# Kernel optimization log

Measured on AMD Instinct MI355X. Metric: run time of the kernel, lower is better.

## Reference

```python
import jax, jax.numpy as jnp
import numpy as np

B, C, H, W = 8, 64, 64, 64
CQ = C // 8  # query/key channels


def setup_inputs() -> dict:
    key = jax.random.key(0)
    ks = jax.random.split(key, 7)
    s = 0.05
    return {
        "x": jax.random.normal(ks[0], (B, C, H, W), jnp.float32),
        "wq": jax.random.normal(ks[1], (CQ, C), jnp.float32) * s,
        "bq": jnp.zeros((CQ,), jnp.float32),
        "wk": jax.random.normal(ks[2], (CQ, C), jnp.float32) * s,
        "bk": jnp.zeros((CQ,), jnp.float32),
        "wv": jax.random.normal(ks[3], (C, C), jnp.float32) * s,
        "bv": jnp.zeros((C,), jnp.float32),
    }


def reference(x, wq, bq, wk, bk, wv, bv):
    b, c, h, w = x.shape
    n = h * w
    xf = x.reshape(b, c, n)                       # [B, C, N]
    # 1x1 convs == per-pixel linear over channels
    q = jnp.einsum('oc,bcn->bon', wq, xf) + bq[None, :, None]   # [B, CQ, N]
    k = jnp.einsum('oc,bcn->bon', wk, xf) + bk[None, :, None]   # [B, CQ, N]
    v = jnp.einsum('oc,bcn->bon', wv, xf) + bv[None, :, None]   # [B, C, N]
    # energy[b, i, j] = q[b, :, i] . k[b, :, j]  (unscaled)
    energy = jnp.einsum('bci,bcj->bij', q, k)     # [B, N, N]
    attention = jax.nn.softmax(energy, axis=-1)   # softmax over j
    # out[b, c, i] = sum_j v[b, c, j] * attention[b, i, j]
    out = jnp.einsum('bcj,bij->bci', v, attention)
    return out.reshape(b, c, h, w)
```

## Files before the change

kernel.cpp:

```cpp
#include <hip/hip_runtime.h>
#include <hip/hip_bf16.h>


#define B_   8
#define C_   64
#define N_   4096
#define LOG2E 1.44269504088896340736f

typedef short bf16x8 __attribute__((ext_vector_type(8)));
typedef float f32x4  __attribute__((ext_vector_type(4)));
typedef unsigned int uint32;

#if __has_builtin(__builtin_amdgcn_exp2f)
#define EXP2(x) __builtin_amdgcn_exp2f(x)
#else
#define EXP2(x) __expf((x) * 0.69314718055994530942f)
#endif

__device__ __forceinline__ unsigned short f2bf_rn(float f) {
    union { __hip_bfloat16 h; unsigned short u; } cv;
    cv.h = __float2bfloat16(f);
    return cv.u;
}
__device__ __forceinline__ uint32 pk_rn(float lo, float hi) {
    return (uint32)f2bf_rn(lo) | ((uint32)f2bf_rn(hi) << 16);
}
__device__ __forceinline__ uint32 pack_rtz(float lo, float hi) {
    return __builtin_amdgcn_perm(__float_as_uint(hi), __float_as_uint(lo), 0x07060302);
}

__global__ __launch_bounds__(256) void prep_kernel(
    const float* __restrict__ x,
    const float* __restrict__ wq, const float* __restrict__ bq,
    const float* __restrict__ wk, const float* __restrict__ bk,
    unsigned short* __restrict__ Qh, unsigned short* __restrict__ Kh,
    unsigned short* __restrict__ Xb)
{
    __shared__ float Xs[C_][64];
    __shared__ float Wqk[16][C_];
    __shared__ float Bqk[16];

    const int t  = threadIdx.x;
    const int b  = blockIdx.x >> 6;
    const int p0 = (blockIdx.x & 63) << 6;

    for (int i = t; i < 1024; i += 256) {
        int o = i >> 6;
        Wqk[o][i & 63] = (o < 8) ? wq[i] * LOG2E : wk[i - 512];
    }
    if (t < 16) Bqk[t] = (t < 8) ? bq[t] * LOG2E : bk[t - 8];

    for (int i = t; i < 2048; i += 256) {
        int c = i >> 5, p2 = (i & 31) << 1;
        const float* xp = x + ((size_t)b * C_ + c) * N_ + p0 + p2;
        float2 v = *(const float2*)xp;
        Xs[c][p2] = v.x; Xs[c][p2 + 1] = v.y;
        *(uint32*)(Xb + ((size_t)b * C_ + c) * N_ + p0 + p2) = pk_rn(v.x, v.y);
    }
    __syncthreads();

    const int pix = t & 63, grp = t >> 6;
    float a[4];
    #pragma unroll
    for (int r = 0; r < 4; ++r) a[r] = Bqk[grp * 4 + r];
    for (int c = 0; c < C_; ++c) {
        float xv = Xs[c][pix];
        #pragma unroll
        for (int r = 0; r < 4; ++r) a[r] += Wqk[grp * 4 + r][c] * xv;
    }
    #pragma unroll
    for (int r = 0; r < 4; ++r) {
        int o = grp * 4 + r;
        unsigned short hv = f2bf_rn(a[r]);
        if (o < 8) Qh[((size_t)b * N_ + p0 + pix) * 8 + o] = hv;
        else       Kh[((size_t)b * N_ + p0 + pix) * 8 + (o - 8)] = hv;
    }
}

__global__ __launch_bounds__(512, 4) void attn_mfma9_kernel(
    const unsigned short* __restrict__ Qh,
    const unsigned short* __restrict__ Kh,
    const unsigned short* __restrict__ Xb,
    const float* __restrict__ wv, const float* __restrict__ bv,
    float* __restrict__ out)
{
    __shared__ __align__(16) char smem[67584];

    const int t    = threadIdx.x;
    const int w    = t >> 6;
    const int lane = t & 63;
    const int l16  = lane & 15;
    const int qd   = lane >> 4;
    const int p    = w & 3;
    const int h    = w >> 2;
    const int b    = blockIdx.x >> 6;
    const int i0   = (blockIdx.x & 63) << 6;

    const bf16x8 z8 = {};
    const f32x4  zf = {};

    bf16x8 qf[4];
    #pragma unroll
    for (int qt = 0; qt < 4; ++qt) {
        qf[qt] = z8;
        if (qd == 0)
            qf[qt] = *(const bf16x8*)(Qh + ((size_t)b * N_ + i0 + qt * 16 + l16) * 8);
    }

    const unsigned short* Kp = Kh + ((size_t)b * N_ + p * 1024 + h * 16) * 8;
    const unsigned short* Xp = Xb + ((size_t)b * C_ + h * 32) * N_ + p * 1024;

    f32x4 acc[2][4];
    #pragma unroll
    for (int ct = 0; ct < 2; ++ct)
        #pragma unroll
        for (int qt = 0; qt < 4; ++qt) acc[ct][qt] = zf;
    float dsum[4] = {0.f, 0.f, 0.f, 0.f};

    const int swz   = (l16 & 3) << 2;
    const int pbase = p * 8192 + l16 * 64;
    const int woff  = ((h * 8 + qd * 2) ^ swz) << 2;
    const int roff  = ((qd * 4) ^ swz) << 2;

    bf16x8 kf[2], xf[2][2];
    kf[0] = z8;
    if (qd == 0) kf[0] = *(const bf16x8*)(Kp + (size_t)l16 * 8);
    #pragma unroll
    for (int ct = 0; ct < 2; ++ct)
        xf[0][ct] = *(const bf16x8*)(Xp + (size_t)(ct * 16 + l16) * N_ + qd * 8);

    #pragma unroll 2
    for (int s = 0; s < 32; ++s) {
        const int cur = s & 1, nxt = cur ^ 1;
        const int jb = s * 32;
        char* pb_ = smem + pbase + cur * 4096;

        f32x4 sf[4];
        #pragma unroll
        for (int qt = 0; qt < 4; ++qt)
            sf[qt] = __builtin_amdgcn_mfma_f32_16x16x32_bf16(kf[cur], qf[qt], zf, 0, 0, 0);

        if (s < 31) {
            bf16x8 nk = z8;
            if (qd == 0) nk = *(const bf16x8*)(Kp + (size_t)(jb + 32 + l16) * 8);
            kf[nxt] = nk;
            #pragma unroll
            for (int ct = 0; ct < 2; ++ct)
                xf[nxt][ct] = *(const bf16x8*)(Xp + (size_t)(ct * 16 + l16) * N_ + jb + 32 + qd * 8);
        }

        #pragma unroll
        for (int qt = 0; qt < 4; ++qt) {
            float e0 = EXP2(sf[qt][0]);
            float e1 = EXP2(sf[qt][1]);
            float e2 = EXP2(sf[qt][2]);
            float e3 = EXP2(sf[qt][3]);
            dsum[qt] += (e0 + e1) + (e2 + e3);
            uint2 u;
            u.x = pack_rtz(e0, e1);
            u.y = pack_rtz(e2, e3);
            *(uint2*)(pb_ + qt * 1024 + woff) = u;
        }

        __syncthreads();

        #pragma unroll
        for (int qt = 0; qt < 4; ++qt) {
            bf16x8 pbf = *(const bf16x8*)(pb_ + qt * 1024 + roff);
            #pragma unroll
            for (int ct = 0; ct < 2; ++ct)
                acc[ct][qt] = __builtin_amdgcn_mfma_f32_16x16x32_bf16(xf[cur][ct], pbf, acc[ct][qt], 0, 0, 0);
        }
    }

    #pragma unroll
    for (int qt = 0; qt < 4; ++qt) {
        float v = dsum[qt];
        v += __shfl_xor(v, 16, 64);
        v += __shfl_xor(v, 32, 64);
        if (qd == 0) *(float*)(smem + 65536 + (w * 64 + qt * 16 + l16) * 4) = v;
    }

    __syncthreads();
    if (p != 0) {
        const int slot = h * 3 + (p - 1);
        char* rb = smem + slot * 8192;
        #pragma unroll
        for (int ct = 0; ct < 2; ++ct)
            #pragma unroll
            for (int qt = 0; qt < 4; ++qt)
                *(f32x4*)(rb + (ct * 4 + qt) * 1024 + lane * 16) = acc[ct][qt];
    }
    __syncthreads();
    if (p == 0) {
        #pragma unroll
        for (int rr = 0; rr < 3; ++rr) {
            const char* rb = smem + (h * 3 + rr) * 8192;
            #pragma unroll
            for (int ct = 0; ct < 2; ++ct)
                #pragma unroll
                for (int qt = 0; qt < 4; ++qt)
                    acc[ct][qt] += *(const f32x4*)(rb + (ct * 4 + qt) * 1024 + lane * 16);
        }
        float* Or = (float*)(smem + 49152);
        #pragma unroll
        for (int ct = 0; ct < 2; ++ct)
            #pragma unroll
            for (int qt = 0; qt < 4; ++qt)
                #pragma unroll
                for (int r = 0; r < 4; ++r)
                    Or[(h * 32 + ct * 16 + qd * 4 + r) * 64 + qt * 16 + l16] = acc[ct][qt][r];
    }
    __syncthreads();
    {
        float* Wvs = (float*)smem;
        for (int i = t; i < 4096; i += 512) Wvs[i] = wv[i];
    }
    __syncthreads();

    const int q = t & 63, grp = t >> 6;
    const float* Wvs = (const float*)smem;
    const float* Or  = (const float*)(smem + 49152);
    const float* Dn  = (const float*)(smem + 65536);
    float dtot = 0.f;
    #pragma unroll
    for (int r = 0; r < 8; ++r) dtot += Dn[r * 64 + q];
    const float inv = 1.0f / dtot;
    float o[8];
    #pragma unroll
    for (int r = 0; r < 8; ++r) o[r] = 0.f;
    for (int k = 0; k < 64; ++k) {
        float ov = Or[k * 64 + q];
        #pragma unroll
        for (int r = 0; r < 8; ++r)
            o[r] += Wvs[(grp * 8 + r) * 64 + k] * ov;
    }
    #pragma unroll
    for (int r = 0; r < 8; ++r)
        out[((size_t)b * C_ + grp * 8 + r) * N_ + i0 + q] = o[r] * inv + bv[grp * 8 + r];
}

__global__ __launch_bounds__(256) void attn_fused_fallback(
    const float* __restrict__ x,
    const float* __restrict__ wq, const float* __restrict__ bq,
    const float* __restrict__ wk, const float* __restrict__ bk,
    const float* __restrict__ wv, const float* __restrict__ bv,
    float* __restrict__ out)
{
    __shared__ float Qs[64][8];
    __shared__ float Ks[8][64];
    __shared__ float Vs[64][C_];
    __shared__ float Ws[64][64 + 1];
    __shared__ float Xs[C_ * 64];
    __shared__ float Wks[8][C_];
    __shared__ float Wvs[C_][C_ + 1];

    const int t     = threadIdx.x;
    const int b     = blockIdx.x / (N_ / 64);
    const int i0    = (blockIdx.x % (N_ / 64)) * 64;
    const int jlane = t & 63;
    const int wgrp  = t >> 6;

    for (int l = t; l < 8 * C_;  l += 256) Wks[l >> 6][l & 63] = wk[l];
    for (int l = t; l < C_ * C_; l += 256) Wvs[l >> 6][l & 63] = wv[l];
    for (int l = t; l < C_ * 64; l += 256)
        Xs[(l >> 6) * 64 + (l & 63)] = x[((size_t)b * C_ + (l >> 6)) * N_ + i0 + (l & 63)];
    __syncthreads();
    {
        int qi = jlane;
        #pragma unroll
        for (int r = 0; r < 2; ++r) {
            int cc = wgrp * 2 + r;
            float a = bq[cc];
            for (int c = 0; c < C_; ++c) a += wq[cc * C_ + c] * Xs[c * 64 + qi];
            Qs[qi][cc] = a;
        }
    }
    __syncthreads();

    const int qi2 = t >> 2;
    const int cb  = (t & 3) << 4;
    float accv[16];
    #pragma unroll
    for (int r = 0; r < 16; ++r) accv[r] = 0.f;
    float denom = 0.f;

    for (int j0 = 0; j0 < N_; j0 += 64) {
        for (int l = t; l < C_ * 64; l += 256)
            Xs[(l >> 6) * 64 + (l & 63)] = x[((size_t)b * C_ + (l >> 6)) * N_ + j0 + (l & 63)];
        __syncthreads();
        {
            int j = jlane;
            #pragma unroll
            for (int r = 0; r < 2; ++r) {
                int cc = wgrp * 2 + r;
                float a = bk[cc];
                for (int c = 0; c < C_; ++c) a += Wks[cc][c] * Xs[c * 64 + j];
                Ks[cc][j] = a;
            }
        }
        {
            int vc = jlane;
            #pragma unroll 2
            for (int r = 0; r < 16; ++r) {
                int j = wgrp * 16 + r;
                float a = bv[vc];
                for (int c = 0; c < C_; ++c) a += Wvs[vc][c] * Xs[c * 64 + j];
                Vs[j][vc] = a;
            }
        }
        __syncthreads();
        {
            float kreg[8];
            #pragma unroll
            for (int cc = 0; cc < 8; ++cc) kreg[cc] = Ks[cc][jlane];
            #pragma unroll 4
            for (int r = 0; r < 16; ++r) {
                int qi = wgrp * 16 + r;
                float e = 0.f;
                #pragma unroll
                for (int cc = 0; cc < 8; ++cc) e += Qs[qi][cc] * kreg[cc];
                Ws[qi][jlane] = __expf(e);
            }
        }
        __syncthreads();
        #pragma unroll 4
        for (int j = 0; j < 64; ++j) {
            float wv2 = Ws[qi2][j];
            denom += wv2;
            const float4* vrow = (const float4*)(&Vs[j][cb]);
            float4 v0 = vrow[0], v1 = vrow[1], v2 = vrow[2], v3 = vrow[3];
            accv[0]  += wv2 * v0.x; accv[1]  += wv2 * v0.y; accv[2]  += wv2 * v0.z; accv[3]  += wv2 * v0.w;
            accv[4]  += wv2 * v1.x; accv[5]  += wv2 * v1.y; accv[6]  += wv2 * v1.z; accv[7]  += wv2 * v1.w;
            accv[8]  += wv2 * v2.x; accv[9]  += wv2 * v2.y; accv[10] += wv2 * v2.z; accv[11] += wv2 * v2.w;
            accv[12] += wv2 * v3.x; accv[13] += wv2 * v3.y; accv[14] += wv2 * v3.z; accv[15] += wv2 * v3.w;
        }
        __syncthreads();
    }

    const float inv = 1.0f / denom;
    #pragma unroll
    for (int r = 0; r < 16; ++r)
        out[((size_t)b * C_ + cb + r) * N_ + i0 + qi2] = accv[r] * inv;
}

extern "C" void kernel_launch(void* const* d_in, const int* in_sizes, int n_in,
                              void* d_out, int out_size, void* d_ws, size_t ws_size,
                              hipStream_t stream)
{
    const float* x  = (const float*)d_in[0];
    const float* wq = (const float*)d_in[1];
    const float* bq = (const float*)d_in[2];
    const float* wk = (const float*)d_in[3];
    const float* bk = (const float*)d_in[4];
    const float* wv = (const float*)d_in[5];
    const float* bv = (const float*)d_in[6];
    float* out = (float*)d_out;

    const size_t nQ = (size_t)B_ * N_ * 8;
    const size_t nX = (size_t)B_ * C_ * N_;
    const size_t needed = (2 * nQ + nX) * sizeof(unsigned short);

    if (ws_size >= needed) {
        unsigned short* Qh = (unsigned short*)d_ws;
        unsigned short* Kh = Qh + nQ;
        unsigned short* Xb = Kh + nQ;
        prep_kernel<<<B_ * (N_ / 64), 256, 0, stream>>>(x, wq, bq, wk, bk, Qh, Kh, Xb);
        attn_mfma9_kernel<<<B_ * (N_ / 64), 512, 0, stream>>>(Qh, Kh, Xb, wv, bv, out);
    } else {
        attn_fused_fallback<<<B_ * (N_ / 64), 256, 0, stream>>>(x, wq, bq, wk, bk, wv, bv, out);
    }
}
```

Before: 123.9 us.

## Process 64 keys per pipeline step to halve block barriers

Widens each main-loop iteration from 32 to 64 keys. Each half-wave group now computes 32 scores per step into a larger double-buffered LDS probability tile, and the PV MFMA stage consumes two 32-key chunks. This halves the number of __syncthreads and loop iterations and gives more independent MFMA work per barrier. The cost is twice as many prefetched K/X fragments held in registers, which under the 512x4 launch bounds risks register pressure or spills.

Measured after the change: 254.0 us. +105.1%, slower.

```diff
diff --git a/kernel.cpp b/kernel.cpp
--- a/kernel.cpp
+++ b/kernel.cpp
@@ -77,7 +77,7 @@
     }
 }
 
-__global__ __launch_bounds__(512, 4) void attn_mfma9_kernel(
+__global__ __launch_bounds__(512, 4) void attn_mfma10_kernel(
     const unsigned short* __restrict__ Qh,
     const unsigned short* __restrict__ Kh,
     const unsigned short* __restrict__ Xb,
@@ -107,7 +107,7 @@
             qf[qt] = *(const bf16x8*)(Qh + ((size_t)b * N_ + i0 + qt * 16 + l16) * 8);
     }
 
-    const unsigned short* Kp = Kh + ((size_t)b * N_ + p * 1024 + h * 16) * 8;
+    const unsigned short* Kp = Kh + ((size_t)b * N_ + p * 1024 + h * 32) * 8;
     const unsigned short* Xp = Xb + ((size_t)b * C_ + h * 32) * N_ + p * 1024;
 
     f32x4 acc[2][4];
@@ -118,59 +118,77 @@
     float dsum[4] = {0.f, 0.f, 0.f, 0.f};
 
     const int swz   = (l16 & 3) << 2;
-    const int pbase = p * 8192 + l16 * 64;
-    const int woff  = ((h * 8 + qd * 2) ^ swz) << 2;
-    const int roff  = ((qd * 4) ^ swz) << 2;
-
-    bf16x8 kf[2], xf[2][2];
-    kf[0] = z8;
-    if (qd == 0) kf[0] = *(const bf16x8*)(Kp + (size_t)l16 * 8);
-    #pragma unroll
-    for (int ct = 0; ct < 2; ++ct)
-        xf[0][ct] = *(const bf16x8*)(Xp + (size_t)(ct * 16 + l16) * N_ + qd * 8);
+    const int pbase = p * 16384 + l16 * 64;
+    int woff[2];
+    #pragma unroll
+    for (int jt = 0; jt < 2; ++jt) woff[jt] = ((jt * 8 + qd * 2) ^ swz) << 2;
+    const int roff = ((qd * 4) ^ swz) << 2;
+
+    bf16x8 kf[2][2], xf[2][2][2];
+    #pragma unroll
+    for (int jt = 0; jt < 2; ++jt) {
+        kf[0][jt] = z8;
+        if (qd == 0) kf[0][jt] = *(const bf16x8*)(Kp + (size_t)(jt * 16 + l16) * 8);
+    }
+    #pragma unroll
+    for (int kc = 0; kc < 2; ++kc)
+        #pragma unroll
+        for (int ct = 0; ct < 2; ++ct)
+            xf[0][kc][ct] = *(const bf16x8*)(Xp + (size_t)(ct * 16 + l16) * N_ + kc * 32 + qd * 8);
 
     #pragma unroll 2
-    for (int s = 0; s < 32; ++s) {
+    for (int s = 0; s < 16; ++s) {
         const int cur = s & 1, nxt = cur ^ 1;
-        const int jb = s * 32;
-        char* pb_ = smem + pbase + cur * 4096;
-
-        f32x4 sf[4];
-        #pragma unroll
-        for (int qt = 0; qt < 4; ++qt)
-            sf[qt] = __builtin_amdgcn_mfma_f32_16x16x32_bf16(kf[cur], qf[qt], zf, 0, 0, 0);
-
-        if (s < 31) {
-            bf16x8 nk = z8;
-            if (qd == 0) nk = *(const bf16x8*)(Kp + (size_t)(jb + 32 + l16) * 8);
-            kf[nxt] = nk;
-            #pragma unroll
-            for (int ct = 0; ct < 2; ++ct)
-                xf[nxt][ct] = *(const bf16x8*)(Xp + (size_t)(ct * 16 + l16) * N_ + jb + 32 + qd * 8);
-        }
-
-        #pragma unroll
-        for (int qt = 0; qt < 4; ++qt) {
-            float e0 = EXP2(sf[qt][0]);
-            float e1 = EXP2(sf[qt][1]);
-            float e2 = EXP2(sf[qt][2]);
-            float e3 = EXP2(sf[qt][3]);
-            dsum[qt] += (e0 + e1) + (e2 + e3);
-            uint2 u;
-            u.x = pack_rtz(e0, e1);
-            u.y = pack_rtz(e2, e3);
-            *(uint2*)(pb_ + qt * 1024 + woff) = u;
-        }
-
-        __syncthreads();
-
-        #pragma unroll
-        for (int qt = 0; qt < 4; ++qt) {
-            bf16x8 pbf = *(const bf16x8*)(pb_ + qt * 1024 + roff);
-            #pragma unroll
-            for (int ct = 0; ct < 2; ++ct)
-                acc[ct][qt] = __builtin_amdgcn_mfma_f32_16x16x32_bf16(xf[cur][ct], pbf, acc[ct][qt], 0, 0, 0);
-        }
+        const int jb = s * 64;
+        char* pb_ = smem + pbase + cur * 8192;
+        char* ps_ = pb_ + h * 4096;
+
+        #pragma unroll
+        for (int jt = 0; jt < 2; ++jt) {
+            f32x4 sf[4];
+            #pragma unroll
+            for (int qt = 0; qt < 4; ++qt)
+                sf[qt] = __builtin_amdgcn_mfma_f32_16x16x32_bf16(kf[cur][jt], qf[qt], zf, 0, 0, 0);
+
+            if (jt == 1 && s < 15) {
+                #pragma unroll
+                for (int j2 = 0; j2 < 2; ++j2) {
+                    bf16x8 nk = z8;
+                    if (qd == 0) nk = *(const bf16x8*)(Kp + (size_t)(jb + 64 + j2 * 16 + l16) * 8);
+                    kf[nxt][j2] = nk;
+                }
+                #pragma unroll
+                for (int kc = 0; kc < 2; ++kc)
+                    #pragma unroll
+                    for (int ct = 0; ct < 2; ++ct)
+                        xf[nxt][kc][ct] = *(const bf16x8*)(Xp + (size_t)(ct * 16 + l16) * N_ + jb + 64 + kc * 32 + qd * 8);
+            }
+
+            #pragma unroll
+            for (int qt = 0; qt < 4; ++qt) {
+                float e0 = EXP2(sf[qt][0]);
+                float e1 = EXP2(sf[qt][1]);
+                float e2 = EXP2(sf[qt][2]);
+                float e3 = EXP2(sf[qt][3]);
+                dsum[qt] += (e0 + e1) + (e2 + e3);
+                uint2 u;
+                u.x = pack_rtz(e0, e1);
+                u.y = pack_rtz(e2, e3);
+                *(uint2*)(ps_ + qt * 1024 + woff[jt]) = u;
+            }
+        }
+
+        __syncthreads();
+
+        #pragma unroll
+        for (int kc = 0; kc < 2; ++kc)
+            #pragma unroll
+            for (int qt = 0; qt < 4; ++qt) {
+                bf16x8 pbf = *(const bf16x8*)(pb_ + kc * 4096 + qt * 1024 + roff);
+                #pragma unroll
+                for (int ct = 0; ct < 2; ++ct)
+                    acc[ct][qt] = __builtin_amdgcn_mfma_f32_16x16x32_bf16(xf[cur][kc][ct], pbf, acc[ct][qt], 0, 0, 0);
+            }
     }
 
     #pragma unroll
@@ -366,7 +384,7 @@
         unsigned short* Kh = Qh + nQ;
         unsigned short* Xb = Kh + nQ;
         prep_kernel<<<B_ * (N_ / 64), 256, 0, stream>>>(x, wq, bq, wk, bk, Qh, Kh, Xb);
-        attn_mfma9_kernel<<<B_ * (N_ / 64), 512, 0, stream>>>(Qh, Kh, Xb, wv, bv, out);
+        attn_mfma10_kernel<<<B_ * (N_ / 64), 512, 0, stream>>>(Qh, Kh, Xb, wv, bv, out);
     } else {
         attn_fused_fallback<<<B_ * (N_ / 64), 256, 0, stream>>>(x, wq, bq, wk, bk, wv, bv, out);
     }
```
